# Kernel tuning notes

Measured on AMD Instinct MI355X. Metric: run time of the kernel, lower is better.

## Reference

```python
import jax, jax.numpy as jnp
import numpy as np

B, T, D = 4, 4096, 1024

def setup_inputs() -> dict:
    key = jax.random.key(0)
    ks = jax.random.split(key, 8)
    s = 1.0 / np.sqrt(D)
    return {
        "x": jax.random.normal(ks[0], (B, T, D), dtype=jnp.float32),
        # diagonal SSM params (per-channel)
        "A": jax.random.uniform(ks[1], (D,), dtype=jnp.float32, minval=0.5, maxval=0.99),  # stable decay
        "Bp": jax.random.normal(ks[2], (D,), dtype=jnp.float32) * 0.1,
        "Cp": jax.random.normal(ks[3], (D,), dtype=jnp.float32),
        # gate Linear
        "gate_w": jax.random.uniform(ks[4], (D, D), dtype=jnp.float32, minval=-s, maxval=s),
        "gate_b": jnp.zeros((D,), dtype=jnp.float32),
        # out Linear
        "out_w": jax.random.uniform(ks[5], (D, D), dtype=jnp.float32, minval=-s, maxval=s),
        "out_b": jnp.zeros((D,), dtype=jnp.float32),
    }

def _ssm(x, A, Bp, Cp):
    # diagonal linear recurrence: h_t = A*h_{t-1} + Bp*x_t ; y_t = Cp*h_t
    bx = x * Bp  # (B,T,D)
    def step(h, bx_t):
        h = A * h + bx_t  # (B,D)
        return h, h
    h0 = jnp.zeros((x.shape[0], x.shape[2]), dtype=x.dtype)
    _, hs = jax.lax.scan(step, h0, jnp.swapaxes(bx, 0, 1))  # (T,B,D)
    return jnp.swapaxes(hs, 0, 1) * Cp  # (B,T,D)

def reference(x, A, Bp, Cp, gate_w, gate_b, out_w, out_b):
    ssm_out = _ssm(x, A, Bp, Cp)
    gate = jax.nn.sigmoid(jnp.einsum('btd,ed->bte', x, gate_w) + gate_b)
    y = gate * ssm_out
    return jnp.einsum('btd,ed->bte', y, out_w) + out_b
```

## Files before the change

kernel.cpp:

```cpp
#include <hip/hip_runtime.h>
#include <hip/hip_bf16.h>
#include <cstdio>

typedef __hip_bfloat16 bf16;
typedef __bf16 bf16x8 __attribute__((ext_vector_type(8)));
typedef float f32x4 __attribute__((ext_vector_type(4)));

#define B_DIM 4
#define T_DIM 4096
#define D_DIM 1024
#define NC 64
#define LC 64

#define M_DIM (B_DIM * T_DIM)
#define BM 256
#define BN 256
#define BK 32
#define NT (D_DIM / BK)
#define GM (M_DIM / BM)
#define GN (D_DIM / BN)

static __device__ __forceinline__ float bfbits2f(unsigned short u) {
  return __uint_as_float(((unsigned)u) << 16);
}
static __device__ __forceinline__ unsigned short f2bfbits(float f) {
  bf16 v = __float2bfloat16(f);
  return *reinterpret_cast<unsigned short*>(&v);
}

__global__ __launch_bounds__(256) void cast_w_kernel(
    const float* __restrict__ gw, const float* __restrict__ ow,
    bf16* __restrict__ gw16, bf16* __restrict__ ow16, int n) {
  int i = blockIdx.x * 256 + threadIdx.x;
  if (i < n) {
    gw16[i] = __float2bfloat16(gw[i]);
    ow16[i] = __float2bfloat16(ow[i]);
  }
}

__global__ __launch_bounds__(256) void ssm_pass1(
    const float* __restrict__ x, const float* __restrict__ A,
    const float* __restrict__ Bp, float* __restrict__ hfin,
    unsigned short* __restrict__ x16) {
  const int tid  = threadIdx.x;
  const int half = blockIdx.x & 1;
  const int c    = (blockIdx.x >> 1) & (NC - 1);
  const int b    = blockIdx.x >> 7;
  const int d0   = half * 512 + tid * 2;
  const float a0 = A[d0], a1 = A[d0 + 1];
  const float bp0 = Bp[d0], bp1 = Bp[d0 + 1];
  const size_t base = (size_t)(b * T_DIM + c * LC) * D_DIM + d0;
  float h0 = 0.f, h1 = 0.f;
#pragma unroll 4
  for (int i = 0; i < LC; ++i) {
    const size_t o = base + (size_t)i * D_DIM;
    const float2 xv = *reinterpret_cast<const float2*>(x + o);
    const unsigned short u0 = f2bfbits(xv.x), u1 = f2bfbits(xv.y);
    const float f0 = bfbits2f(u0), f1 = bfbits2f(u1);
    h0 = fmaf(a0, h0, bp0 * f0);
    h1 = fmaf(a1, h1, bp1 * f1);
    *reinterpret_cast<ushort2*>(x16 + o) = make_ushort2(u0, u1);
  }
  const int ho = (b * NC + c) * D_DIM + d0;
  hfin[ho] = h0;
  hfin[ho + 1] = h1;
}

__global__ __launch_bounds__(256) void ssm_pass2(
    const float* __restrict__ A, const float* __restrict__ hfin,
    float* __restrict__ hin) {
  const int idx = blockIdx.x * 256 + threadIdx.x;
  const int d = idx & (D_DIM - 1);
  const int b = idx >> 10;
  float aL = A[d];
#pragma unroll
  for (int s = 0; s < 6; ++s) aL *= aL;
  float h = 0.f;
  for (int c = 0; c < NC; ++c) {
    const int o = (b * NC + c) * D_DIM + d;
    hin[o] = h;
    h = fmaf(aL, h, hfin[o]);
  }
}

__global__ __launch_bounds__(256) void ssm_pass3(
    const unsigned short* __restrict__ x16, const float* __restrict__ A,
    const float* __restrict__ Bp, const float* __restrict__ Cp,
    const float* __restrict__ hin, unsigned short* __restrict__ ssm16) {
  const int tid  = threadIdx.x;
  const int half = blockIdx.x & 1;
  const int c    = (blockIdx.x >> 1) & (NC - 1);
  const int b    = blockIdx.x >> 7;
  const int d0   = half * 512 + tid * 2;
  const float a0 = A[d0], a1 = A[d0 + 1];
  const float bp0 = Bp[d0], bp1 = Bp[d0 + 1];
  const float cp0 = Cp[d0], cp1 = Cp[d0 + 1];
  const int ho = (b * NC + c) * D_DIM + d0;
  float h0 = hin[ho], h1 = hin[ho + 1];
  const size_t base = (size_t)(b * T_DIM + c * LC) * D_DIM + d0;
#pragma unroll 4
  for (int i = 0; i < LC; ++i) {
    const size_t o = base + (size_t)i * D_DIM;
    const ushort2 u = *reinterpret_cast<const ushort2*>(x16 + o);
    h0 = fmaf(a0, h0, bp0 * bfbits2f(u.x));
    h1 = fmaf(a1, h1, bp1 * bfbits2f(u.y));
    *reinterpret_cast<ushort2*>(ssm16 + o) =
        make_ushort2(f2bfbits(cp0 * h0), f2bfbits(cp1 * h1));
  }
}

template <bool GATE>
__global__ __launch_bounds__(512) void gemm256(
    const bf16* __restrict__ Xm, const bf16* __restrict__ Wm,
    const float* __restrict__ bias, const bf16* __restrict__ ssm,
    bf16* __restrict__ Ybf, float* __restrict__ Yf) {
  __shared__ __align__(16) short LDS[4][16384];

  const int tid  = threadIdx.x;
  const int lane = tid & 63;
  const int wave = tid >> 6;
  const int wm = wave >> 2;
  const int wn = wave & 3;
  const int l15 = lane & 15;
  const int sA = ((lane >> 4) ^ ((l15 >> 1) & 3)) << 3;

  const int bid = blockIdx.x;
  const int swz = (bid & 7) * (GM * GN / 8) + (bid >> 3);
  const int m0 = (swz >> 2) * BM;
  const int n0 = (swz & 3) * BN;

  const int row0 = tid >> 2;
  const int c0   = (tid & 3) ^ ((row0 >> 1) & 3);
  const size_t offA0 = (size_t)(m0 + row0) * D_DIM + c0 * 8;
  const size_t offB0 = (size_t)(n0 + row0) * D_DIM + c0 * 8;

  auto gll = [](const bf16* g, short* l) {
    __builtin_amdgcn_global_load_lds(
        (const __attribute__((address_space(1))) void*)g,
        (__attribute__((address_space(3))) void*)l, 16, 0, 0);
  };
  auto STAGE = [&](int buf, int kt) {
    const size_t ko = (size_t)kt * BK;
    short* b0 = &LDS[buf][0] + wave * 512;
    gll(Xm + offA0 + ko,               b0);
    gll(Xm + offA0 + 128 * D_DIM + ko, b0 + 4096);
    gll(Wm + offB0 + ko,               b0 + 8192);
    gll(Wm + offB0 + 128 * D_DIM + ko, b0 + 12288);
  };

  f32x4 acc[8][4] = {};

  STAGE(0, 0);
  STAGE(1, 1);
  STAGE(2, 2);
  asm volatile("s_waitcnt vmcnt(8)" ::: "memory");
  __builtin_amdgcn_s_barrier();

#define KTILE_BODY(T_, VMSTR, DO_STAGE, DO_BAR)                             \
  {                                                                         \
    const short* bb = &LDS[(T_) & 3][0];                                    \
    bf16x8 a[8], b[4];                                                      \
                      \
    _Pragma("unroll")                                                       \
    for (int i = 0; i < 4; ++i)                                             \
      a[i] = *(const bf16x8*)(bb + (wm * 128 + i * 16 + l15) * BK + sA);    \
    _Pragma("unroll")                                                       \
    for (int j = 0; j < 4; ++j)                                             \
      b[j] = *(const bf16x8*)(bb + 8192 + (wn * 64 + j * 16 + l15) * BK + sA); \
    _Pragma("unroll")                                                       \
    for (int i = 4; i < 8; ++i)                                             \
      a[i] = *(const bf16x8*)(bb + (wm * 128 + i * 16 + l15) * BK + sA);    \
    if (DO_STAGE) STAGE(((T_) + 3) & 3, (T_) + 3);                          \
    __builtin_amdgcn_s_setprio(1);                                          \
    _Pragma("unroll")                                                       \
    for (int i = 0; i < 4; ++i)                                             \
      _Pragma("unroll")                                                     \
      for (int j = 0; j < 4; ++j)                                           \
        acc[i][j] =                                                         \
            __builtin_amdgcn_mfma_f32_16x16x32_bf16(a[i], b[j], acc[i][j], 0, 0, 0); \
    __builtin_amdgcn_s_setprio(0);                                          \
    if (DO_BAR) {                                                           \
      asm volatile("s_waitcnt " VMSTR ::: "memory");                        \
      __builtin_amdgcn_s_barrier();                                         \
    }                                                                       \
    __builtin_amdgcn_s_setprio(1);                                          \
    _Pragma("unroll")                                                       \
    for (int i = 4; i < 8; ++i)                                             \
      _Pragma("unroll")                                                     \
      for (int j = 0; j < 4; ++j)                                           \
        acc[i][j] =                                                         \
            __builtin_amdgcn_mfma_f32_16x16x32_bf16(a[i], b[j], acc[i][j], 0, 0, 0); \
    __builtin_amdgcn_s_setprio(0);                                          \
  }

  for (int t = 0; t < NT - 3; ++t)
    KTILE_BODY(t, "vmcnt(8)", true, true);
  KTILE_BODY(NT - 3, "vmcnt(4)", false, true);
  KTILE_BODY(NT - 2, "vmcnt(0)", false, true);
  KTILE_BODY(NT - 1, "vmcnt(0)", false, false);
#undef KTILE_BODY

#pragma unroll
  for (int i = 0; i < 8; ++i) {
#pragma unroll
    for (int j = 0; j < 4; ++j) {
      const int col = n0 + wn * 64 + j * 16 + l15;
      const float bv = bias[col];
#pragma unroll
      for (int v = 0; v < 4; ++v) {
        const int row = m0 + wm * 128 + i * 16 + (lane >> 4) * 4 + v;
        const size_t o = (size_t)row * D_DIM + col;
        const float val = acc[i][j][v] + bv;
        if (GATE) {
          const float g = 1.f / (1.f + expf(-val));
          Ybf[o] = __float2bfloat16(g * __bfloat162float(ssm[o]));
        } else {
          Yf[o] = val;
        }
      }
    }
  }
}

extern "C" void kernel_launch(void* const* d_in, const int* in_sizes, int n_in,
                              void* d_out, int out_size, void* d_ws, size_t ws_size,
                              hipStream_t stream) {
  const float* x  = (const float*)d_in[0];
  const float* A  = (const float*)d_in[1];
  const float* Bp = (const float*)d_in[2];
  const float* Cp = (const float*)d_in[3];
  const float* gw = (const float*)d_in[4];
  const float* gb = (const float*)d_in[5];
  const float* ow = (const float*)d_in[6];
  const float* ob = (const float*)d_in[7];
  float* out = (float*)d_out;

  const size_t NEED = 73400320;
  if (ws_size < NEED) {
    fprintf(stderr, "kernel_launch: ws_size %zu < needed %zu\n", ws_size, NEED);
    return;
  }
  char* ws = (char*)d_ws;
  bf16*  x16   = (bf16*)(ws);
  bf16*  ssm16 = (bf16*)(ws + 33554432);
  bf16*  gw16  = (bf16*)(ws + 67108864);
  bf16*  ow16  = (bf16*)(ws + 69206016);
  float* hfin  = (float*)(ws + 71303168);
  float* hin   = (float*)(ws + 72351744);

  cast_w_kernel<<<(D_DIM * D_DIM) / 256, 256, 0, stream>>>(gw, ow, gw16, ow16, D_DIM * D_DIM);
  ssm_pass1<<<B_DIM * NC * 2, 256, 0, stream>>>(x, A, Bp, hfin,
                                                (unsigned short*)x16);
  ssm_pass2<<<(B_DIM * D_DIM) / 256, 256, 0, stream>>>(A, hfin, hin);
  ssm_pass3<<<B_DIM * NC * 2, 256, 0, stream>>>((const unsigned short*)x16, A,
                                                Bp, Cp, hin,
                                                (unsigned short*)ssm16);

  gemm256<true><<<GM * GN, 512, 0, stream>>>(x16, gw16, gb, ssm16, ssm16, nullptr);
  gemm256<false><<<GM * GN, 512, 0, stream>>>(ssm16, ow16, ob, nullptr, nullptr, out);
}
```

Before: 127.8 us.

## Fuse SSM chunk-scan pass into gated GEMM prologue

Removes the separate ssm_pass3 kernel and recomputes each 256x256 tile's SSM outputs inside the gate GEMM's prologue. The scan runs after the first three K-tiles are staged, so it overlaps with those loads. Each thread scans 64 timesteps for one channel, reading x and writing ssm with scalar 2-byte accesses. The goal is to save a kernel launch and keep the ssm tile in cache for the epilogue. The cost is a serialized 64-step latency-bound loop before the GEMM main loop, plus a full vmcnt(0) wait in place of vmcnt(8).

```diff
diff --git a/kernel.cpp b/kernel.cpp
--- a/kernel.cpp
+++ b/kernel.cpp
@@ -83,37 +83,14 @@
   }
 }
 
-__global__ __launch_bounds__(256) void ssm_pass3(
-    const unsigned short* __restrict__ x16, const float* __restrict__ A,
-    const float* __restrict__ Bp, const float* __restrict__ Cp,
-    const float* __restrict__ hin, unsigned short* __restrict__ ssm16) {
-  const int tid  = threadIdx.x;
-  const int half = blockIdx.x & 1;
-  const int c    = (blockIdx.x >> 1) & (NC - 1);
-  const int b    = blockIdx.x >> 7;
-  const int d0   = half * 512 + tid * 2;
-  const float a0 = A[d0], a1 = A[d0 + 1];
-  const float bp0 = Bp[d0], bp1 = Bp[d0 + 1];
-  const float cp0 = Cp[d0], cp1 = Cp[d0 + 1];
-  const int ho = (b * NC + c) * D_DIM + d0;
-  float h0 = hin[ho], h1 = hin[ho + 1];
-  const size_t base = (size_t)(b * T_DIM + c * LC) * D_DIM + d0;
-#pragma unroll 4
-  for (int i = 0; i < LC; ++i) {
-    const size_t o = base + (size_t)i * D_DIM;
-    const ushort2 u = *reinterpret_cast<const ushort2*>(x16 + o);
-    h0 = fmaf(a0, h0, bp0 * bfbits2f(u.x));
-    h1 = fmaf(a1, h1, bp1 * bfbits2f(u.y));
-    *reinterpret_cast<ushort2*>(ssm16 + o) =
-        make_ushort2(f2bfbits(cp0 * h0), f2bfbits(cp1 * h1));
-  }
-}
-
 template <bool GATE>
 __global__ __launch_bounds__(512) void gemm256(
     const bf16* __restrict__ Xm, const bf16* __restrict__ Wm,
     const float* __restrict__ bias, const bf16* __restrict__ ssm,
-    bf16* __restrict__ Ybf, float* __restrict__ Yf) {
+    bf16* __restrict__ Ybf, float* __restrict__ Yf,
+    const unsigned short* __restrict__ x16s, const float* __restrict__ Ap,
+    const float* __restrict__ Bpp, const float* __restrict__ Cpp,
+    const float* __restrict__ hinp) {
   __shared__ __align__(16) short LDS[4][16384];
 
   const int tid  = threadIdx.x;
@@ -153,7 +130,29 @@
   STAGE(0, 0);
   STAGE(1, 1);
   STAGE(2, 2);
-  asm volatile("s_waitcnt vmcnt(8)" ::: "memory");
+
+  if (GATE) {
+    unsigned short* ssms = (unsigned short*)ssm;
+    const int bb_   = m0 >> 12;
+    const int cbase = (m0 & 4095) >> 6;
+#pragma unroll
+    for (int p = 0; p < 2; ++p) {
+      const int idx = p * 512 + tid;
+      const int ch  = idx & 255;
+      const int ck  = idx >> 8;
+      const int d   = n0 + ch;
+      const float a = Ap[d], bp = Bpp[d], cp = Cpp[d];
+      float h = hinp[(bb_ * NC + cbase + ck) * D_DIM + d];
+      size_t o = (size_t)(m0 + ck * 64) * D_DIM + d;
+#pragma unroll 8
+      for (int i = 0; i < LC; ++i, o += D_DIM) {
+        h = fmaf(a, h, bp * bfbits2f(x16s[o]));
+        ssms[o] = f2bfbits(cp * h);
+      }
+    }
+  }
+
+  asm volatile("s_waitcnt vmcnt(0)" ::: "memory");
   __builtin_amdgcn_s_barrier();
 
 #define KTILE_BODY(T_, VMSTR, DO_STAGE, DO_BAR)                             \
@@ -252,10 +251,11 @@
   ssm_pass1<<<B_DIM * NC * 2, 256, 0, stream>>>(x, A, Bp, hfin,
                                                 (unsigned short*)x16);
   ssm_pass2<<<(B_DIM * D_DIM) / 256, 256, 0, stream>>>(A, hfin, hin);
-  ssm_pass3<<<B_DIM * NC * 2, 256, 0, stream>>>((const unsigned short*)x16, A,
-                                                Bp, Cp, hin,
-                                                (unsigned short*)ssm16);
-
-  gemm256<true><<<GM * GN, 512, 0, stream>>>(x16, gw16, gb, ssm16, ssm16, nullptr);
-  gemm256<false><<<GM * GN, 512, 0, stream>>>(ssm16, ow16, ob, nullptr, nullptr, out);
-}
+
+  gemm256<true><<<GM * GN, 512, 0, stream>>>(
+      x16, gw16, gb, ssm16, ssm16, nullptr,
+      (const unsigned short*)x16, A, Bp, Cp, hin);
+  gemm256<false><<<GM * GN, 512, 0, stream>>>(
+      ssm16, ow16, ob, nullptr, nullptr, out,
+      nullptr, nullptr, nullptr, nullptr, nullptr);
+}
```

After: 126.7 us. No clear change (-0.9%).
